# Optimization experiments

Hardware: AMD Instinct MI355X
Metric: run time of the kernel (lower is better)

Reference implementation:

```python
import jax, jax.numpy as jnp
import numpy as np

HEAD_NUM = 16


def setup_inputs() -> dict:
    key = jax.random.key(0)
    k1, k2, k3, k4 = jax.random.split(key, 4)
    B, S, E = 8, 1024, 1024
    inputs = jax.random.normal(k1, (B, S, E), dtype=jnp.float32)
    W_Query = jax.random.normal(k2, (E, E), dtype=jnp.float32) * 0.05
    W_Key = jax.random.normal(k3, (E, E), dtype=jnp.float32) * 0.05
    W_Value = jax.random.normal(k4, (E, E), dtype=jnp.float32) * 0.05
    return {"inputs": inputs, "W_Query": W_Query, "W_Key": W_Key, "W_Value": W_Value}


def reference(inputs, W_Query, W_Key, W_Value):
    B, S, E = inputs.shape
    H = HEAD_NUM
    D = E // H
    # QKV projections: [B,S,E] @ [E,E] -> [B,S,E]
    q = jnp.einsum('bse,ef->bsf', inputs, W_Query).reshape(B, S, H, D)
    k = jnp.einsum('bse,ef->bsf', inputs, W_Key).reshape(B, S, H, D)
    v = jnp.einsum('bse,ef->bsf', inputs, W_Value).reshape(B, S, H, D)
    # NOTE: original has NO 1/sqrt(D) scaling.
    scores = jnp.einsum('bihd,bjhd->bhij', q, k)  # [B,H,S,S]
    att = jax.nn.softmax(scores, axis=-1)
    out = jnp.einsum('bhij,bjhd->bihd', att, v).reshape(B, S, E)
    return jax.nn.relu(out)
```

## Files before the change

kernel.cpp:

```cpp
#include <hip/hip_runtime.h>
#include <cstdint>
#include <cstddef>

#define B_ 8
#define S_ 1024
#define E_ 1024
#define H_ 16
#define D_ 64
#define M_ (B_*S_)

typedef _Float16 f16;
typedef __attribute__((ext_vector_type(8))) _Float16 f16x8;
typedef __attribute__((ext_vector_type(4))) _Float16 f16x4;
typedef __attribute__((ext_vector_type(4))) float  f32x4;
typedef __attribute__((ext_vector_type(16))) float f32x16;
typedef __attribute__((ext_vector_type(4))) int    int4v;
typedef __attribute__((ext_vector_type(2))) int    int2v;

__device__ __forceinline__ f32x4 mfma16(f16x8 a, f16x8 b, f32x4 c) {
  return __builtin_amdgcn_mfma_f32_16x16x32_f16(a, b, c, 0, 0, 0);
}
__device__ __forceinline__ f32x16 mfma32(f16x8 a, f16x8 b, f32x16 c) {
  return __builtin_amdgcn_mfma_f32_32x32x16_f16(a, b, c, 0, 0, 0);
}
__device__ __forceinline__ void gll16(const f16* g, f16* l) {
  __builtin_amdgcn_global_load_lds(
      (const __attribute__((address_space(1))) void*)g,
      (__attribute__((address_space(3))) void*)l, 16, 0, 0);
}
__device__ __forceinline__ int pkrtz(float lo, float hi) {
  return __builtin_bit_cast(int, __builtin_amdgcn_cvt_pkrtz(lo, hi));
}

__global__ __launch_bounds__(256) void presplit_kernel(
    const float* __restrict__ X, f16* __restrict__ Xf) {
  size_t i = ((size_t)blockIdx.x * 256 + threadIdx.x) * 8;
  f32x4 v0 = *(const f32x4*)&X[i];
  f32x4 v1 = *(const f32x4*)&X[i + 4];
  f16x8 hv;
#pragma unroll
  for (int j = 0; j < 4; ++j) {
    hv[j] = (f16)v0[j];
    hv[j + 4] = (f16)v1[j];
  }
  *(f16x8*)&Xf[i] = hv;
}

__global__ __launch_bounds__(512) void wt_conv3_kernel(
    const float* __restrict__ Wq, const float* __restrict__ Wk,
    const float* __restrict__ Wv, f16* __restrict__ oq, f16* __restrict__ ok,
    f16* __restrict__ ov) {
  const float* W = blockIdx.z == 0 ? Wq : (blockIdx.z == 1 ? Wk : Wv);
  f16* o = blockIdx.z == 0 ? oq : (blockIdx.z == 1 ? ok : ov);
  const float scl = blockIdx.z == 0 ? 1.4426950408889634f : 1.0f;
  __shared__ float t[64][65];
  const int f0 = blockIdx.x * 64, e0 = blockIdx.y * 64;
  const int tx = threadIdx.x, ty = threadIdx.y;
#pragma unroll
  for (int j = 0; j < 8; ++j)
    t[ty + 8 * j][tx] = W[(size_t)(e0 + ty + 8 * j) * E_ + f0 + tx];
  __syncthreads();
#pragma unroll
  for (int j = 0; j < 8; ++j)
    o[(size_t)(f0 + ty + 8 * j) * E_ + e0 + tx] =
        (f16)(t[tx][ty + 8 * j] * scl);
}

__global__ __launch_bounds__(256) void gemm_qkv_kernel(
    const f16* __restrict__ Xf,
    const f16* __restrict__ Wq, const f16* __restrict__ Wk,
    const f16* __restrict__ Wv,
    f16* __restrict__ Qh, f16* __restrict__ Ql,
    f16* __restrict__ Kf, f16* __restrict__ Vt) {
  __shared__ f16 sA[128][64], sB[128][64];
  const int bid = blockIdx.x;
  const int xcd = bid & 7, idx = bid >> 3;
  const int mb = xcd * 8 + idx / 24;
  const int nb = idx % 24;
  const int z = nb >> 3;
  const int n0 = (nb & 7) * 128, m0 = mb * 128;
  const f16* __restrict__ Bt = z == 0 ? Wq : (z == 1 ? Wk : Wv);
  const int tid = threadIdx.x;
  const int lane = tid & 63, w = tid >> 6;
  const int wm = (w >> 1) * 64, wn = (w & 1) * 64;
  const int fr = lane & 15, fg = lane >> 4;
  f32x4 acc[4][4] = {};
  for (int k0 = 0; k0 < E_; k0 += 64) {
#pragma unroll
    for (int i = 0; i < 4; ++i) {
      int ci = tid + i * 256;
      int r = ci >> 3, cl = ci & 7;
      int cs = (cl ^ (r & 7)) * 8;
      gll16(Xf + (size_t)(m0 + r) * E_ + k0 + cs, &sA[0][0] + ci * 8);
      gll16(Bt + (size_t)(n0 + r) * E_ + k0 + cs, &sB[0][0] + ci * 8);
    }
    __syncthreads();
#pragma unroll
    for (int kh2 = 0; kh2 < 2; ++kh2) {
      f16x8 ah[4];
#pragma unroll
      for (int mi = 0; mi < 4; ++mi) {
        int rA = wm + mi * 16 + fr;
        ah[mi] = *(const f16x8*)&sA[rA][(((kh2 * 4 + fg) ^ (rA & 7))) * 8];
      }
#pragma unroll
      for (int ni = 0; ni < 4; ++ni) {
        int rB = wn + ni * 16 + fr;
        f16x8 bh = *(const f16x8*)&sB[rB][(((kh2 * 4 + fg) ^ (rB & 7))) * 8];
#pragma unroll
        for (int mi = 0; mi < 4; ++mi)
          acc[mi][ni] = mfma16(ah[mi], bh, acc[mi][ni]);
      }
    }
    __syncthreads();
  }
  if (z == 0) {
#pragma unroll
    for (int mi = 0; mi < 4; ++mi)
#pragma unroll
      for (int ni = 0; ni < 4; ++ni)
#pragma unroll
        for (int r = 0; r < 4; ++r) {
          int row = m0 + wm + mi * 16 + (lane >> 4) * 4 + r;
          int col = n0 + wn + ni * 16 + fr;
          float v = acc[mi][ni][r];
          int bb = row >> 10, s = row & 1023;
          int hd = col >> 6, d = col & 63;
          size_t idx2 = ((size_t)(bb * H_ + hd) * S_ + s) * D_ + d;
          f16 hh = (f16)v;
          Qh[idx2] = hh;
          Ql[idx2] = (f16)(v - (float)hh);
        }
  } else if (z == 1) {
#pragma unroll
    for (int mi = 0; mi < 4; ++mi)
#pragma unroll
      for (int ni = 0; ni < 4; ++ni)
#pragma unroll
        for (int r = 0; r < 4; ++r) {
          int row = m0 + wm + mi * 16 + (lane >> 4) * 4 + r;
          int col = n0 + wn + ni * 16 + fr;
          int bb = row >> 10, s = row & 1023;
          int hd = col >> 6, d = col & 63;
          Kf[((size_t)(bb * H_ + hd) * S_ + s) * D_ + d] = (f16)acc[mi][ni][r];
        }
  } else {
#pragma unroll
    for (int mi = 0; mi < 4; ++mi)
#pragma unroll
      for (int ni = 0; ni < 4; ++ni) {
        int row = m0 + wm + mi * 16 + (lane >> 4) * 4;
        int col = n0 + wn + ni * 16 + fr;
        int bb = row >> 10, s = row & 1023;
        int hd = col >> 6, d = col & 63;
        f16x4 p;
#pragma unroll
        for (int r = 0; r < 4; ++r) p[r] = (f16)acc[mi][ni][r];
        *(f16x4*)&Vt[((size_t)(bb * H_ + hd) * D_ + d) * S_ + s] = p;
      }
  }
}

__global__ __launch_bounds__(256, 2) void attn_kernel(
    const f16* __restrict__ Qh, const f16* __restrict__ Ql,
    const f16* __restrict__ Kf, const f16* __restrict__ Vt,
    float* __restrict__ out) {
  __shared__ f16 sK[3][64][64], sV[3][64][64];
  const int bid = blockIdx.x;
  const int idx = bid >> 3;
  const int bh = (bid & 7) * 16 + (idx >> 2);
  const int qb = idx & 3;
  const int hd = bh & 15, bb = bh >> 4;
  const int tid = threadIdx.x;
  const int lane = tid & 63, w = tid >> 6;
  const int cq = lane & 31, h = lane >> 5;
  const int rsw = cq & 7;
  const size_t base = (size_t)bh * (S_ * D_);
  const f16* Qh_p = Qh + base;
  const f16* Ql_p = Ql + base;
  const f16* Kf_p = Kf + base;
  const f16* Vt_p = Vt + base;
  const int q0 = qb * 256 + w * 64;

  f16x8 qh_[2][4], ql_[2][4];
#pragma unroll
  for (int qf = 0; qf < 2; ++qf)
#pragma unroll
    for (int ks = 0; ks < 4; ++ks) {
      size_t off = (size_t)(q0 + qf * 32 + cq) * D_ + ks * 16 + 8 * h;
      qh_[qf][ks] = *(const f16x8*)&Qh_p[off];
      ql_[qf][ks] = *(const f16x8*)&Ql_p[off];
    }

  float m_run[2], l_run[2];
  f32x16 O[2][2] = {};
  f16x8 pf[2][4];

#define STAGE(buf, kb)                                                        \
  {                                                                           \
    _Pragma("unroll")                                                         \
    for (int half = 0; half < 2; ++half) {                                    \
      int ci = tid + half * 256;                                              \
      int row = ci >> 3, cl = ci & 7;                                         \
      int cs = cl ^ (row & 7);                                                \
      gll16(Kf_p + (size_t)((kb) + row) * D_ + cs * 8, &sK[buf][0][0] + ci * 8); \
      gll16(Vt_p + (size_t)row * S_ + (kb) + cs * 8, &sV[buf][0][0] + ci * 8);   \
    }                                                                         \
  }

#define QKT(scv, bufi)                                                        \
  {                                                                           \
    _Pragma("unroll")                                                         \
    for (int f = 0; f < 2; ++f) {                                             \
      _Pragma("unroll")                                                       \
      for (int ks = 0; ks < 4; ++ks) {                                        \
        int cc = ((2 * ks + h) ^ rsw) * 8;                                    \
        f16x8 kv = *(const f16x8*)&sK[bufi][f * 32 + cq][cc];                 \
        _Pragma("unroll")                                                     \
        for (int qf = 0; qf < 2; ++qf) {                                      \
          scv[qf][f] = mfma32(kv, qh_[qf][ks], scv[qf][f]);                   \
          scv[qf][f] = mfma32(kv, ql_[qf][ks], scv[qf][f]);                   \
        }                                                                     \
      }                                                                       \
    }                                                                         \
  }

#define PVT(bufi)                                                             \
  {                                                                           \
    _Pragma("unroll")                                                         \
    for (int ks = 0; ks < 4; ++ks) {                                          \
      _Pragma("unroll")                                                       \
      for (int df = 0; df < 2; ++df) {                                        \
        int cc = ((2 * ks + h) ^ rsw) * 8;                                    \
        f16x8 vf = *(const f16x8*)&sV[bufi][df * 32 + cq][cc];                \
        O[0][df] = mfma32(vf, pf[0][ks], O[0][df]);                           \
        O[1][df] = mfma32(vf, pf[1][ks], O[1][df]);                           \
      }                                                                       \
    }                                                                         \
  }

#define PFBUILD(qf, scv)                                                      \
  {                                                                           \
    _Pragma("unroll")                                                         \
    for (int f = 0; f < 2; ++f) {                                             \
      _Pragma("unroll")                                                       \
      for (int ksl = 0; ksl < 2; ++ksl) {                                     \
        int b0 = 8 * ksl;                                                     \
        int a1 = pkrtz(scv[qf][f][b0 + 0], scv[qf][f][b0 + 1]);               \
        int b1 = pkrtz(scv[qf][f][b0 + 4], scv[qf][f][b0 + 5]);               \
        int2v r1 = __builtin_amdgcn_permlane32_swap(a1, b1, false, false);    \
        int a2 = pkrtz(scv[qf][f][b0 + 2], scv[qf][f][b0 + 3]);               \
        int b2 = pkrtz(scv[qf][f][b0 + 6], scv[qf][f][b0 + 7]);               \
        int2v r2 = __builtin_amdgcn_permlane32_swap(a2, b2, false, false);    \
        int4v wd;                                                             \
        wd[0] = r1[0]; wd[1] = r2[0]; wd[2] = r1[1]; wd[3] = r2[1];           \
        pf[qf][2 * f + ksl] = __builtin_bit_cast(f16x8, wd);                  \
      }                                                                       \
    }                                                                         \
  }

#define MAXTREE(pm, scv, qf)                                                  \
  {                                                                           \
    float t4[4];                                                              \
    _Pragma("unroll")                                                         \
    for (int i = 0; i < 4; ++i) {                                             \
      float a = fmaxf(fmaxf(scv[qf][0][i], scv[qf][0][i + 4]),                \
                      fmaxf(scv[qf][0][i + 8], scv[qf][0][i + 12]));          \
      float b = fmaxf(fmaxf(scv[qf][1][i], scv[qf][1][i + 4]),                \
                      fmaxf(scv[qf][1][i + 8], scv[qf][1][i + 12]));          \
      t4[i] = fmaxf(a, b);                                                    \
    }                                                                         \
    pm = fmaxf(fmaxf(t4[0], t4[1]), fmaxf(t4[2], t4[3]));                     \
    pm = fmaxf(pm, __shfl_xor(pm, 32));                                       \
  }

#define ROWSUM(rs, scv, qf)                                                   \
  {                                                                           \
    float rs0 = 0.f, rs1 = 0.f, rs2 = 0.f, rs3 = 0.f;                         \
    _Pragma("unroll")                                                         \
    for (int f = 0; f < 2; ++f) {                                             \
      _Pragma("unroll")                                                       \
      for (int r4 = 0; r4 < 4; ++r4) {                                        \
        rs0 += scv[qf][f][4 * r4 + 0];                                        \
        rs1 += scv[qf][f][4 * r4 + 1];                                        \
        rs2 += scv[qf][f][4 * r4 + 2];                                        \
        rs3 += scv[qf][f][4 * r4 + 3];                                        \
      }                                                                       \
    }                                                                         \
    rs = (rs0 + rs1) + (rs2 + rs3);                                           \
    rs += __shfl_xor(rs, 32);                                                 \
  }

  int bc = 0, bn = 1, bs = 2;
  STAGE(0, 0);
  asm volatile("s_waitcnt vmcnt(0)" ::: "memory");
  __builtin_amdgcn_sched_barrier(0);
  __builtin_amdgcn_s_barrier();
  STAGE(1, 64);
  {
    f32x16 sc[2][2] = {};
    QKT(sc, 0);
#pragma unroll
    for (int qf = 0; qf < 2; ++qf) {
      float pm;
      MAXTREE(pm, sc, qf);
      m_run[qf] = pm;
#pragma unroll
      for (int f = 0; f < 2; ++f)
#pragma unroll
        for (int r = 0; r < 16; ++r)
          sc[qf][f][r] = __builtin_amdgcn_exp2f(sc[qf][f][r] - pm);
      float rs;
      ROWSUM(rs, sc, qf);
      l_run[qf] = rs;
      PFBUILD(qf, sc);
    }
  }

  for (int t = 0; t < 15; ++t) {
    asm volatile("s_waitcnt vmcnt(0)" ::: "memory");
    __builtin_amdgcn_sched_barrier(0);
    __builtin_amdgcn_s_barrier();

    f32x16 sc[2][2];
#pragma unroll
    for (int qf = 0; qf < 2; ++qf)
#pragma unroll
      for (int f = 0; f < 2; ++f)
#pragma unroll
        for (int r = 0; r < 16; ++r) sc[qf][f][r] = -m_run[qf];
    __builtin_amdgcn_s_setprio(1);
    QKT(sc, bn);
    __builtin_amdgcn_s_setprio(0);
    if (t < 14) STAGE(bs, (t + 2) * 64);

#pragma unroll
    for (int qf = 0; qf < 2; ++qf)
#pragma unroll
      for (int f = 0; f < 2; ++f)
#pragma unroll
        for (int r = 0; r < 16; ++r)
          sc[qf][f][r] = __builtin_amdgcn_exp2f(sc[qf][f][r]);
    float pm0, pm1;
    MAXTREE(pm0, sc, 0);
    MAXTREE(pm1, sc, 1);
    bool trig = __any(fmaxf(pm0, pm1) > 2048.f);
    float scl[2] = {1.f, 1.f};
    if (trig) {
#pragma unroll
      for (int qf = 0; qf < 2; ++qf) {
        float pmx = fmaxf(qf == 0 ? pm0 : pm1, 1.0f);
        scl[qf] = 1.0f / pmx;
        m_run[qf] += __builtin_amdgcn_logf(pmx);
#pragma unroll
        for (int f = 0; f < 2; ++f)
#pragma unroll
          for (int r = 0; r < 16; ++r) sc[qf][f][r] *= scl[qf];
      }
    }

    __builtin_amdgcn_s_setprio(1);
    PVT(bc);
    __builtin_amdgcn_s_setprio(0);

    if (trig) {
#pragma unroll
      for (int qf = 0; qf < 2; ++qf) {
        l_run[qf] *= scl[qf];
#pragma unroll
        for (int df = 0; df < 2; ++df)
#pragma unroll
          for (int i = 0; i < 16; ++i) O[qf][df][i] *= scl[qf];
      }
    }
#pragma unroll
    for (int qf = 0; qf < 2; ++qf) {
      float rs;
      ROWSUM(rs, sc, qf);
      l_run[qf] += rs;
      PFBUILD(qf, sc);
    }
    int tmp = bc; bc = bn; bn = bs; bs = tmp;
  }
  PVT(bc);

#pragma unroll
  for (int qf = 0; qf < 2; ++qf) {
    float inv = 1.0f / l_run[qf];
    int s = q0 + qf * 32 + cq;
    float* orow = out + ((size_t)bb * S_ + s) * E_ + hd * 64;
#pragma unroll
    for (int df = 0; df < 2; ++df)
#pragma unroll
      for (int g = 0; g < 4; ++g) {
        f32x4 vv;
#pragma unroll
        for (int j = 0; j < 4; ++j)
          vv[j] = fmaxf(O[qf][df][4 * g + j] * inv, 0.f);
        *(f32x4*)&orow[df * 32 + 8 * g + 4 * h] = vv;
      }
  }
}

extern "C" void kernel_launch(void* const* d_in, const int* in_sizes, int n_in,
                              void* d_out, int out_size, void* d_ws, size_t ws_size,
                              hipStream_t stream) {
  const float* X  = (const float*)d_in[0];
  const float* Wq = (const float*)d_in[1];
  const float* Wk = (const float*)d_in[2];
  const float* Wv = (const float*)d_in[3];
  float* out = (float*)d_out;
  char* ws = (char*)d_ws;

  const size_t WSZ = (size_t)E_ * E_ * sizeof(f16);
  const size_t QSZ = (size_t)M_ * E_ * sizeof(f16);
  f16* Wqf = (f16*)(ws);
  f16* Wkf = (f16*)(ws + WSZ);
  f16* Wvf = (f16*)(ws + 2 * WSZ);
  char* p = ws + 3 * WSZ;
  f16* Xf = (f16*)(p);
  f16* Qh = (f16*)(p + QSZ);
  f16* Ql = (f16*)(p + 2 * QSZ);
  f16* Kf = (f16*)(p + 3 * QSZ);
  f16* Vt = (f16*)(p + 4 * QSZ);

  presplit_kernel<<<4096, 256, 0, stream>>>(X, Xf);
  wt_conv3_kernel<<<dim3(16, 16, 3), dim3(64, 8), 0, stream>>>(
      Wq, Wk, Wv, Wqf, Wkf, Wvf);

  gemm_qkv_kernel<<<1536, 256, 0, stream>>>(
      Xf, Wqf, Wkf, Wvf, Qh, Ql, Kf, Vt);

  attn_kernel<<<512, 256, 0, stream>>>(Qh, Ql, Kf, Vt, out);
}
```

Before: 159.2 us.

## Halve per-wave query rows in attention to double grid and raise occupancy

Each wave now processes 32 query rows instead of 64, so the attention grid doubles to 1024 blocks and launch bounds allow 3 blocks per CU. Per-thread register state (Q fragments, O accumulators, scores) is halved, which is meant to improve occupancy and latency hiding. In exchange, each K/V tile staged in LDS is reused by fewer queries, which doubles K/V global traffic, and the grid may leave a partial wave of blocks.

```diff
diff --git a/kernel.cpp b/kernel.cpp
--- a/kernel.cpp
+++ b/kernel.cpp
@@ -161,15 +161,14 @@
   }
 }
 
-__global__ __launch_bounds__(256, 2) void attn_kernel(
+__global__ __launch_bounds__(256, 3) void attn_kernel(
     const f16* __restrict__ Qh, const f16* __restrict__ Ql,
     const f16* __restrict__ Kf, const f16* __restrict__ Vt,
     float* __restrict__ out) {
   __shared__ f16 sK[3][64][64], sV[3][64][64];
   const int bid = blockIdx.x;
-  const int idx = bid >> 3;
-  const int bh = (bid & 7) * 16 + (idx >> 2);
-  const int qb = idx & 3;
+  const int bh = (bid & 7) * 16 + (bid >> 6);
+  const int qb = (bid >> 3) & 7;
   const int hd = bh & 15, bb = bh >> 4;
   const int tid = threadIdx.x;
   const int lane = tid & 63, w = tid >> 6;
@@ -180,21 +179,19 @@
   const f16* Ql_p = Ql + base;
   const f16* Kf_p = Kf + base;
   const f16* Vt_p = Vt + base;
-  const int q0 = qb * 256 + w * 64;
-
-  f16x8 qh_[2][4], ql_[2][4];
-#pragma unroll
-  for (int qf = 0; qf < 2; ++qf)
-#pragma unroll
-    for (int ks = 0; ks < 4; ++ks) {
-      size_t off = (size_t)(q0 + qf * 32 + cq) * D_ + ks * 16 + 8 * h;
-      qh_[qf][ks] = *(const f16x8*)&Qh_p[off];
-      ql_[qf][ks] = *(const f16x8*)&Ql_p[off];
-    }
-
-  float m_run[2], l_run[2];
-  f32x16 O[2][2] = {};
-  f16x8 pf[2][4];
+  const int q0 = qb * 128 + w * 32;
+
+  f16x8 qh_[4], ql_[4];
+#pragma unroll
+  for (int ks = 0; ks < 4; ++ks) {
+    size_t off = (size_t)(q0 + cq) * D_ + ks * 16 + 8 * h;
+    qh_[ks] = *(const f16x8*)&Qh_p[off];
+    ql_[ks] = *(const f16x8*)&Ql_p[off];
+  }
+
+  float m_run, l_run;
+  f32x16 O[2] = {};
+  f16x8 pf[4];
 
 #define STAGE(buf, kb)                                                        \
   {                                                                           \
@@ -216,11 +213,8 @@
       for (int ks = 0; ks < 4; ++ks) {                                        \
         int cc = ((2 * ks + h) ^ rsw) * 8;                                    \
         f16x8 kv = *(const f16x8*)&sK[bufi][f * 32 + cq][cc];                 \
-        _Pragma("unroll")                                                     \
-        for (int qf = 0; qf < 2; ++qf) {                                      \
-          scv[qf][f] = mfma32(kv, qh_[qf][ks], scv[qf][f]);                   \
-          scv[qf][f] = mfma32(kv, ql_[qf][ks], scv[qf][f]);                   \
-        }                                                                     \
+        scv[f] = mfma32(kv, qh_[ks], scv[f]);                                 \
+        scv[f] = mfma32(kv, ql_[ks], scv[f]);                                 \
       }                                                                       \
     }                                                                         \
   }
@@ -233,58 +227,57 @@
       for (int df = 0; df < 2; ++df) {                                        \
         int cc = ((2 * ks + h) ^ rsw) * 8;                                    \
         f16x8 vf = *(const f16x8*)&sV[bufi][df * 32 + cq][cc];                \
-        O[0][df] = mfma32(vf, pf[0][ks], O[0][df]);                           \
-        O[1][df] = mfma32(vf, pf[1][ks], O[1][df]);                           \
+        O[df] = mfma32(vf, pf[ks], O[df]);                                    \
       }                                                                       \
     }                                                                         \
   }
 
-#define PFBUILD(qf, scv)                                                      \
+#define PFBUILD(scv)                                                          \
   {                                                                           \
     _Pragma("unroll")                                                         \
     for (int f = 0; f < 2; ++f) {                                             \
       _Pragma("unroll")                                                       \
       for (int ksl = 0; ksl < 2; ++ksl) {                                     \
         int b0 = 8 * ksl;                                                     \
-        int a1 = pkrtz(scv[qf][f][b0 + 0], scv[qf][f][b0 + 1]);               \
-        int b1 = pkrtz(scv[qf][f][b0 + 4], scv[qf][f][b0 + 5]);               \
+        int a1 = pkrtz(scv[f][b0 + 0], scv[f][b0 + 1]);                       \
+        int b1 = pkrtz(scv[f][b0 + 4], scv[f][b0 + 5]);                       \
         int2v r1 = __builtin_amdgcn_permlane32_swap(a1, b1, false, false);    \
-        int a2 = pkrtz(scv[qf][f][b0 + 2], scv[qf][f][b0 + 3]);               \
-        int b2 = pkrtz(scv[qf][f][b0 + 6], scv[qf][f][b0 + 7]);               \
+        int a2 = pkrtz(scv[f][b0 + 2], scv[f][b0 + 3]);                       \
+        int b2 = pkrtz(scv[f][b0 + 6], scv[f][b0 + 7]);                       \
         int2v r2 = __builtin_amdgcn_permlane32_swap(a2, b2, false, false);    \
         int4v wd;                                                             \
         wd[0] = r1[0]; wd[1] = r2[0]; wd[2] = r1[1]; wd[3] = r2[1];           \
-        pf[qf][2 * f + ksl] = __builtin_bit_cast(f16x8, wd);                  \
+        pf[2 * f + ksl] = __builtin_bit_cast(f16x8, wd);                      \
       }                                                                       \
     }                                                                         \
   }
 
-#define MAXTREE(pm, scv, qf)                                                  \
+#define MAXTREE(pm, scv)                                                      \
   {                                                                           \
     float t4[4];                                                              \
     _Pragma("unroll")                                                         \
     for (int i = 0; i < 4; ++i) {                                             \
-      float a = fmaxf(fmaxf(scv[qf][0][i], scv[qf][0][i + 4]),                \
-                      fmaxf(scv[qf][0][i + 8], scv[qf][0][i + 12]));          \
-      float b = fmaxf(fmaxf(scv[qf][1][i], scv[qf][1][i + 4]),                \
-                      fmaxf(scv[qf][1][i + 8], scv[qf][1][i + 12]));          \
+      float a = fmaxf(fmaxf(scv[0][i], scv[0][i + 4]),                        \
+                      fmaxf(scv[0][i + 8], scv[0][i + 12]));                  \
+      float b = fmaxf(fmaxf(scv[1][i], scv[1][i + 4]),                        \
+                      fmaxf(scv[1][i + 8], scv[1][i + 12]));                  \
       t4[i] = fmaxf(a, b);                                                    \
     }                                                                         \
     pm = fmaxf(fmaxf(t4[0], t4[1]), fmaxf(t4[2], t4[3]));                     \
     pm = fmaxf(pm, __shfl_xor(pm, 32));                                       \
   }
 
-#define ROWSUM(rs, scv, qf)                                                   \
+#define ROWSUM(rs, scv)                                                       \
   {                                                                           \
     float rs0 = 0.f, rs1 = 0.f, rs2 = 0.f, rs3 = 0.f;                         \
     _Pragma("unroll")                                                         \
     for (int f = 0; f < 2; ++f) {                                             \
       _Pragma("unroll")                                                       \
       for (int r4 = 0; r4 < 4; ++r4) {                                        \
-        rs0 += scv[qf][f][4 * r4 + 0];                                        \
-        rs1 += scv[qf][f][4 * r4 + 1];                                        \
-        rs2 += scv[qf][f][4 * r4 + 2];                                        \
-        rs3 += scv[qf][f][4 * r4 + 3];                                        \
+        rs0 += scv[f][4 * r4 + 0];                                            \
+        rs1 += scv[f][4 * r4 + 1];                                            \
+        rs2 += scv[f][4 * r4 + 2];                                            \
+        rs3 += scv[f][4 * r4 + 3];                                            \
       }                                                                       \
     }                                                                         \
     rs = (rs0 + rs1) + (rs2 + rs3);                                           \
@@ -298,23 +291,20 @@
   __builtin_amdgcn_s_barrier();
   STAGE(1, 64);
   {
-    f32x16 sc[2][2] = {};
+    f32x16 sc[2] = {};
     QKT(sc, 0);
-#pragma unroll
-    for (int qf = 0; qf < 2; ++qf) {
-      float pm;
-      MAXTREE(pm, sc, qf);
-      m_run[qf] = pm;
-#pragma unroll
-      for (int f = 0; f < 2; ++f)
-#pragma unroll
-        for (int r = 0; r < 16; ++r)
-          sc[qf][f][r] = __builtin_amdgcn_exp2f(sc[qf][f][r] - pm);
-      float rs;
-      ROWSUM(rs, sc, qf);
-      l_run[qf] = rs;
-      PFBUILD(qf, sc);
-    }
+    float pm;
+    MAXTREE(pm, sc);
+    m_run = pm;
+#pragma unroll
+    for (int f = 0; f < 2; ++f)
+#pragma unroll
+      for (int r = 0; r < 16; ++r)
+        sc[f][r] = __builtin_amdgcn_exp2f(sc[f][r] - pm);
+    float rs;
+    ROWSUM(rs, sc);
+    l_run = rs;
+    PFBUILD(sc);
   }
 
   for (int t = 0; t < 15; ++t) {
@@ -322,41 +312,33 @@
     __builtin_amdgcn_sched_barrier(0);
     __builtin_amdgcn_s_barrier();
 
-    f32x16 sc[2][2];
-#pragma unroll
-    for (int qf = 0; qf < 2; ++qf)
-#pragma unroll
-      for (int f = 0; f < 2; ++f)
-#pragma unroll
-        for (int r = 0; r < 16; ++r) sc[qf][f][r] = -m_run[qf];
+    f32x16 sc[2];
+#pragma unroll
+    for (int f = 0; f < 2; ++f)
+#pragma unroll
+      for (int r = 0; r < 16; ++r) sc[f][r] = -m_run;
     __builtin_amdgcn_s_setprio(1);
     QKT(sc, bn);
     __builtin_amdgcn_s_setprio(0);
     if (t < 14) STAGE(bs, (t + 2) * 64);
 
 #pragma unroll
-    for (int qf = 0; qf < 2; ++qf)
+    for (int f = 0; f < 2; ++f)
+#pragma unroll
+      for (int r = 0; r < 16; ++r)
+        sc[f][r] = __builtin_amdgcn_exp2f(sc[f][r]);
+    float pm;
+    MAXTREE(pm, sc);
+    bool trig = __any(pm > 2048.f);
+    float scl = 1.f;
+    if (trig) {
+      float pmx = fmaxf(pm, 1.0f);
+      scl = 1.0f / pmx;
+      m_run += __builtin_amdgcn_logf(pmx);
 #pragma unroll
       for (int f = 0; f < 2; ++f)
 #pragma unroll
-        for (int r = 0; r < 16; ++r)
-          sc[qf][f][r] = __builtin_amdgcn_exp2f(sc[qf][f][r]);
-    float pm0, pm1;
-    MAXTREE(pm0, sc, 0);
-    MAXTREE(pm1, sc, 1);
-    bool trig = __any(fmaxf(pm0, pm1) > 2048.f);
-    float scl[2] = {1.f, 1.f};
-    if (trig) {
-#pragma unroll
-      for (int qf = 0; qf < 2; ++qf) {
-        float pmx = fmaxf(qf == 0 ? pm0 : pm1, 1.0f);
-        scl[qf] = 1.0f / pmx;
-        m_run[qf] += __builtin_amdgcn_logf(pmx);
-#pragma unroll
-        for (int f = 0; f < 2; ++f)
-#pragma unroll
-          for (int r = 0; r < 16; ++r) sc[qf][f][r] *= scl[qf];
-      }
+        for (int r = 0; r < 16; ++r) sc[f][r] *= scl;
     }
 
     __builtin_amdgcn_s_setprio(1);
@@ -364,42 +346,33 @@
     __builtin_amdgcn_s_setprio(0);
 
     if (trig) {
-#pragma unroll
-      for (int qf = 0; qf < 2; ++qf) {
-        l_run[qf] *= scl[qf];
-#pragma unroll
-        for (int df = 0; df < 2; ++df)
-#pragma unroll
-          for (int i = 0; i < 16; ++i) O[qf][df][i] *= scl[qf];
-      }
+      l_run *= scl;
+#pragma unroll
+      for (int df = 0; df < 2; ++df)
+#pragma unroll
+        for (int i = 0; i < 16; ++i) O[df][i] *= scl;
     }
-#pragma unroll
-    for (int qf = 0; qf < 2; ++qf) {
-      float rs;
-      ROWSUM(rs, sc, qf);
-      l_run[qf] += rs;
-      PFBUILD(qf, sc);
+    float rs;
+    ROWSUM(rs, sc);
+    l_run += rs;
+    PFBUILD(sc);
+    int tmp = bc; bc = bn; bn = bs; bs = tmp;
+  }
+  PVT(bc);
+
+  float inv = 1.0f / l_run;
+  int s = q0 + cq;
+  float* orow = out + ((size_t)bb * S_ + s) * E_ + hd * 64;
+#pragma unroll
+  for (int df = 0; df < 2; ++df)
+#pragma unroll
+    for (int g = 0; g < 4; ++g) {
+      f32x4 vv;
+#pragma unroll
+      for (int j = 0; j < 4; ++j)
+        vv[j] = fmaxf(O[df][4 * g + j] * inv, 0.f);
+      *(f32x4*)&orow[df * 32 + 8 * g + 4 * h] = vv;
     }
-    int tmp = bc; bc = bn; bn = bs; bs = tmp;
-  }
-  PVT(bc);
-
-#pragma unroll
-  for (int qf = 0; qf < 2; ++qf) {
-    float inv = 1.0f / l_run[qf];
-    int s = q0 + qf * 32 + cq;
-    float* orow = out + ((size_t)bb * S_ + s) * E_ + hd * 64;
-#pragma unroll
-    for (int df = 0; df < 2; ++df)
-#pragma unroll
-      for (int g = 0; g < 4; ++g) {
-        f32x4 vv;
-#pragma unroll
-        for (int j = 0; j < 4; ++j)
-          vv[j] = fmaxf(O[qf][df][4 * g + j] * inv, 0.f);
-        *(f32x4*)&orow[df * 32 + 8 * g + 4 * h] = vv;
-      }
-  }
 }
 
 extern "C" void kernel_launch(void* const* d_in, const int* in_sizes, int n_in,
@@ -431,5 +404,5 @@
   gemm_qkv_kernel<<<1536, 256, 0, stream>>>(
       Xf, Wqf, Wkf, Wvf, Qh, Ql, Kf, Vt);
 
-  attn_kernel<<<512, 256, 0, stream>>>(Qh, Ql, Kf, Vt, out);
-}
+  attn_kernel<<<1024, 256, 0, stream>>>(Qh, Ql, Kf, Vt, out);
+}
```

After: 147.0 us. -7.7%, faster.
